# Kernel tuning notes

Measured on AMD Instinct MI355X. Metric: run time of the kernel, lower is better.

## Reference

```python
import jax, jax.numpy as jnp
import numpy as np

N4, N3, N2, N1, K = 32768, 65536, 131072, 262144, 16
G = 512


def _w(key, fan_in, fan_out):
    return jax.random.normal(key, (fan_in, fan_out), dtype=jnp.float32) / np.sqrt(fan_in)


def setup_inputs() -> dict:
    key = jax.random.key(0)
    ks = jax.random.split(key, 24)

    def edges(k, n_coarse, n_fine):
        # each fine (output) point gathers from K random coarse (input) points
        src = jax.random.randint(k, (n_fine * K,), 0, n_coarse, dtype=jnp.int32)
        dst = jnp.repeat(jnp.arange(n_fine, dtype=jnp.int32), K)
        return src, dst

    src3, dst3 = edges(ks[0], N4, N3)
    src2, dst2 = edges(ks[1], N3, N2)
    src1, dst1 = edges(ks[2], N2, N1)

    def gidx(k, n):
        return jnp.sort(jax.random.randint(k, (n,), 0, G, dtype=jnp.int32))

    inp = {
        'z_mask': jax.random.normal(ks[3], (N4, 64), dtype=jnp.float32),
        'pos4': jax.random.normal(ks[4], (N4, 3), dtype=jnp.float32),
        'pos3': jax.random.normal(ks[5], (N3, 3), dtype=jnp.float32),
        'pos2': jax.random.normal(ks[6], (N2, 3), dtype=jnp.float32),
        'pos1': jax.random.normal(ks[7], (N1, 3), dtype=jnp.float32),
        'g4': gidx(ks[8], N4), 'g3': gidx(ks[9], N3),
        'g2': gidx(ks[10], N2), 'g1': gidx(ks[11], N1),
        # PointConv MLP params: Linear(c_in+3 -> c_mid), CELU, Linear(c_mid -> c_out), max-aggregate
        'w1a': _w(ks[12], 64 + 3, 64), 'b1a': jnp.zeros((64,), jnp.float32),
        'w1b': _w(ks[13], 64, 32), 'b1b': jnp.zeros((32,), jnp.float32),
        'w2a': _w(ks[14], 32 + 3, 16), 'b2a': jnp.zeros((16,), jnp.float32),
        'w2b': _w(ks[15], 16, 16), 'b2b': jnp.zeros((16,), jnp.float32),
        'w3a': _w(ks[16], 16 + 3, 8), 'b3a': jnp.zeros((8,), jnp.float32),
        'w3b': _w(ks[17], 8, 8), 'b3b': jnp.zeros((8,), jnp.float32),
        'wlin': _w(ks[18], 8, 1), 'blin': jnp.zeros((1,), jnp.float32),
        'src3': src3, 'dst3': dst3,
        'src2': src2, 'dst2': dst2,
        'src1': src1, 'dst1': dst1,
    }
    return inp


def point_conv(x_in, pos_in, pos_out, src, dst, w_a, b_a, w_b, b_b, n_out):
    # gather: per-edge neighbor features + relative positions
    rel = pos_in[src] - pos_out[dst]                      # [E, 3]
    feat = jnp.concatenate([x_in[src], rel], axis=-1)     # [E, c_in+3]
    h = jax.nn.celu(feat @ w_a + b_a)                     # [E, c_mid]
    m = h @ w_b + b_b                                     # [E, c_out]
    # scatter: max-aggregate edge messages onto output points
    return jax.ops.segment_max(m, dst, num_segments=n_out)


def reference(z_mask, pos4, pos3, pos2, pos1, g4, g3, g2, g1,
              w1a, b1a, w1b, b1b, w2a, b2a, w2b, b2b, w3a, b3a, w3b, b3b,
              wlin, blin, src3, dst3, src2, dst2, src1, dst1):
    out = jax.nn.celu(point_conv(z_mask, pos4, pos3, src3, dst3, w1a, b1a, w1b, b1b, N3))
    out = jax.nn.celu(point_conv(out, pos3, pos2, src2, dst2, w2a, b2a, w2b, b2b, N2))
    out = jax.nn.celu(point_conv(out, pos2, pos1, src1, dst1, w3a, b3a, w3b, b3b, N1))
    logits = out @ wlin + blin                            # [N1, 1]
    return jax.nn.log_sigmoid(logits)
```

## Files before the change

kernel.cpp:

```cpp
#include <hip/hip_runtime.h>
#include <hip/hip_fp16.h>
#include <math.h>

#define N4C 32768
#define N3C 65536
#define N2C 131072
#define N1C 262144

typedef _Float16 f16x8 __attribute__((ext_vector_type(8)));
typedef float f32x4 __attribute__((ext_vector_type(4)));
typedef float f32x16 __attribute__((ext_vector_type(16)));

__device__ __forceinline__ f32x4 mfma16(f16x8 a, f16x8 b, f32x4 c) {
  return __builtin_amdgcn_mfma_f32_16x16x32_f16(a, b, c, 0, 0, 0);
}
__device__ __forceinline__ f32x16 mfma32(f16x8 a, f16x8 b, f32x16 c) {
  return __builtin_amdgcn_mfma_f32_32x32x16_f16(a, b, c, 0, 0, 0);
}

__device__ __forceinline__ float celuf(float x) {
  return fmaxf(x, 0.f) + (__expf(fminf(x, 0.f)) - 1.f);
}

__device__ __forceinline__ float logsigf(float x) {
  float e = __expf(-fabsf(x));
  return fminf(x, 0.f) - __logf(1.f + e);
}

__device__ __forceinline__ float max3f(float a, float b, float c) {
  return fmaxf(fmaxf(a, b), c);
}

__device__ __forceinline__ _Float16 exp2_16(_Float16 x) {
  __half h; __builtin_memcpy(&h, &x, 2);
  h = hexp2(h);
  _Float16 r; __builtin_memcpy(&r, &h, 2);
  return r;
}

__device__ __forceinline__ f16x8 celu8p1(f16x8 x) {
  f16x8 z = {};
  f16x8 mx = __builtin_elementwise_max(x, z);
  f16x8 mn = __builtin_elementwise_min(x, z) * (_Float16)1.44269504f;
#pragma unroll
  for (int i = 0; i < 8; ++i) mn[i] = exp2_16(mn[i]);
  return mx + mn;
}

__global__ __launch_bounds__(256) void y4_kernel(
    const float* __restrict__ z, const float* __restrict__ pos4,
    const float* __restrict__ pos3, const float* __restrict__ w1a,
    const float* __restrict__ b1a, _Float16* __restrict__ y4,
    _Float16* __restrict__ vt3) {
  if (blockIdx.x >= 512) {
    const int idx = (blockIdx.x - 512) * 256 + threadIdx.x;
    const int p = idx >> 3, seg = (idx & 7) * 8;
    const float q0 = pos3[p * 3 + 0];
    const float q1 = pos3[p * 3 + 1];
    const float q2 = pos3[p * 3 + 2];
    f16x8 v;
#pragma unroll
    for (int j = 0; j < 8; ++j) {
      const int k = seg + j;
      v[j] = (_Float16)(w1a[64 * 64 + k] * q0 + w1a[65 * 64 + k] * q1 +
                        w1a[66 * 64 + k] * q2);
    }
    *(f16x8*)(vt3 + (size_t)p * 64 + seg) = v;
    return;
  }
  const int lane = threadIdx.x & 63, wid = threadIdx.x >> 6;
  const int col = lane & 15, quad = lane >> 4;
  const int base = (blockIdx.x * 4 + wid) * 16;

  f16x8 Ba[2][4];
#pragma unroll
  for (int c = 0; c < 2; ++c)
#pragma unroll
    for (int t = 0; t < 4; ++t)
#pragma unroll
      for (int j = 0; j < 8; ++j)
        Ba[c][t][j] = (_Float16)w1a[(c * 32 + quad * 8 + j) * 64 + t * 16 + col];

  float wr[3][4];
#pragma unroll
  for (int c = 0; c < 3; ++c)
#pragma unroll
    for (int t = 0; t < 4; ++t)
      wr[c][t] = w1a[(64 + c) * 64 + t * 16 + col];

  float px[4], py[4], pz[4];
#pragma unroll
  for (int r = 0; r < 4; ++r) {
    const int row = base + quad * 4 + r;
    px[r] = pos4[row * 3 + 0];
    py[r] = pos4[row * 3 + 1];
    pz[r] = pos4[row * 3 + 2];
  }

  const float* zr = z + (size_t)(base + col) * 64;
  f16x8 A0, A1;
  {
    float4 f0 = *(const float4*)(zr + quad * 8);
    float4 f1 = *(const float4*)(zr + quad * 8 + 4);
    float4 f2 = *(const float4*)(zr + 32 + quad * 8);
    float4 f3 = *(const float4*)(zr + 32 + quad * 8 + 4);
    A0[0] = (_Float16)f0.x; A0[1] = (_Float16)f0.y; A0[2] = (_Float16)f0.z; A0[3] = (_Float16)f0.w;
    A0[4] = (_Float16)f1.x; A0[5] = (_Float16)f1.y; A0[6] = (_Float16)f1.z; A0[7] = (_Float16)f1.w;
    A1[0] = (_Float16)f2.x; A1[1] = (_Float16)f2.y; A1[2] = (_Float16)f2.z; A1[3] = (_Float16)f2.w;
    A1[4] = (_Float16)f3.x; A1[5] = (_Float16)f3.y; A1[6] = (_Float16)f3.z; A1[7] = (_Float16)f3.w;
  }
#pragma unroll
  for (int t = 0; t < 4; ++t) {
    f32x4 acc = {0.f, 0.f, 0.f, 0.f};
    acc = mfma16(A0, Ba[0][t], acc);
    acc = mfma16(A1, Ba[1][t], acc);
    const float bt = b1a[t * 16 + col];
#pragma unroll
    for (int r = 0; r < 4; ++r) {
      const float posterm =
          px[r] * wr[0][t] + py[r] * wr[1][t] + pz[r] * wr[2][t];
      y4[(size_t)(base + quad * 4 + r) * 64 + t * 16 + col] =
          (_Float16)(acc[r] + bt + posterm);
    }
  }
}

__global__ __launch_bounds__(256) void y3_kernel(
    const _Float16* __restrict__ x3f, const float* __restrict__ pos3,
    const float* __restrict__ pos2, const float* __restrict__ w2a,
    const float* __restrict__ b2a, _Float16* __restrict__ y3,
    _Float16* __restrict__ vt2) {
  if (blockIdx.x >= 1024) {
    const int idx = (blockIdx.x - 1024) * 256 + threadIdx.x;
    const int p = idx >> 1, seg = (idx & 1) * 8;
    const float q0 = pos2[p * 3 + 0];
    const float q1 = pos2[p * 3 + 1];
    const float q2 = pos2[p * 3 + 2];
    f16x8 v;
#pragma unroll
    for (int j = 0; j < 8; ++j) {
      const int k = seg + j;
      v[j] = (_Float16)(w2a[32 * 16 + k] * q0 + w2a[33 * 16 + k] * q1 +
                        w2a[34 * 16 + k] * q2);
    }
    *(f16x8*)(vt2 + (size_t)p * 16 + seg) = v;
    return;
  }
  const int lane = threadIdx.x & 63, wid = threadIdx.x >> 6;
  const int col = lane & 15, quad = lane >> 4;
  const int base = (blockIdx.x * 4 + wid) * 16;

  f16x8 B;
#pragma unroll
  for (int j = 0; j < 8; ++j) B[j] = (_Float16)w2a[(quad * 8 + j) * 16 + col];

  float wr[3];
#pragma unroll
  for (int c = 0; c < 3; ++c) wr[c] = w2a[(32 + c) * 16 + col];

  float px[4], py[4], pz[4];
#pragma unroll
  for (int r = 0; r < 4; ++r) {
    const int row = base + quad * 4 + r;
    px[r] = pos3[row * 3 + 0];
    py[r] = pos3[row * 3 + 1];
    pz[r] = pos3[row * 3 + 2];
  }

  f16x8 A = *(const f16x8*)(x3f + (size_t)(base + col) * 32 + quad * 8);
  f32x4 d = {0.f, 0.f, 0.f, 0.f};
  d = mfma16(A, B, d);
  const float bt = b2a[col];
#pragma unroll
  for (int r = 0; r < 4; ++r) {
    const float posterm = px[r] * wr[0] + py[r] * wr[1] + pz[r] * wr[2];
    y3[(size_t)(base + quad * 4 + r) * 16 + col] =
        (_Float16)(d[r] + bt + posterm);
  }
}

__global__ __launch_bounds__(256) void y2_kernel(
    const _Float16* __restrict__ x2f, const float* __restrict__ pos2,
    const float* __restrict__ pos1, const float* __restrict__ w3a,
    const float* __restrict__ b3a, _Float16* __restrict__ y2,
    _Float16* __restrict__ vt1) {
  if (blockIdx.x >= 2048) {
    const int p = (blockIdx.x - 2048) * 256 + threadIdx.x;
    const float q0 = pos1[p * 3 + 0];
    const float q1 = pos1[p * 3 + 1];
    const float q2 = pos1[p * 3 + 2];
    f16x8 v;
#pragma unroll
    for (int k = 0; k < 8; ++k)
      v[k] = (_Float16)(w3a[16 * 8 + k] * q0 + w3a[17 * 8 + k] * q1 +
                        w3a[18 * 8 + k] * q2);
    *(f16x8*)(vt1 + (size_t)p * 8) = v;
    return;
  }
  const int lane = threadIdx.x & 63, wid = threadIdx.x >> 6;
  const int col = lane & 15, quad = lane >> 4;
  const int base = (blockIdx.x * 4 + wid) * 16;

  f16x8 B;
#pragma unroll
  for (int j = 0; j < 8; ++j) {
    int k = quad * 8 + j;
    B[j] = (k < 16 && col < 8) ? (_Float16)w3a[k * 8 + col] : (_Float16)0.f;
  }
  f16x8 A = *(const f16x8*)(x2f + (size_t)(base + col) * 16 + (quad & 1) * 8);
  f32x4 d = {0.f, 0.f, 0.f, 0.f};
  d = mfma16(A, B, d);
  if (col < 8) {
    float wr[3];
#pragma unroll
    for (int c = 0; c < 3; ++c) wr[c] = w3a[(16 + c) * 8 + col];
    const float bt = b3a[col];
#pragma unroll
    for (int r = 0; r < 4; ++r) {
      const int row = base + quad * 4 + r;
      const float posterm = pos2[row * 3 + 0] * wr[0] +
                            pos2[row * 3 + 1] * wr[1] +
                            pos2[row * 3 + 2] * wr[2];
      y2[(size_t)row * 8 + col] = (_Float16)(d[r] + bt + posterm);
    }
  }
}

__global__ __launch_bounds__(256) void l3_kernel(
    const _Float16* __restrict__ y4, const _Float16* __restrict__ vt3,
    const int* __restrict__ src3, const float* __restrict__ w1b,
    const float* __restrict__ b1b, _Float16* __restrict__ x3f) {
  const int lane = threadIdx.x & 63, wid = threadIdx.x >> 6;
  const int n = lane & 31;
  const int kh = lane >> 5;

  f16x8 Bb[4];
#pragma unroll
  for (int ks = 0; ks < 4; ++ks)
#pragma unroll
    for (int j = 0; j < 8; ++j)
      Bb[ks][j] = (_Float16)w1b[(ks * 16 + kh * 8 + j) * 32 + n];

  float s = 0.f;
#pragma unroll 4
  for (int k = 0; k < 32; ++k) s += w1b[(kh * 32 + k) * 32 + n];
  s += __shfl_xor(s, 32, 64);
  const float biasB = b1b[n] - s;

  const int gwave = blockIdx.x * 4 + wid;
  const int nw = gridDim.x << 2;

#pragma unroll 1
  for (int pb = gwave * 2; pb < N3C; pb += nw * 2) {
    const int s1 = src3[pb * 16 + n];
    const int p = pb + (n >> 4);
    const _Float16* yrow = y4 + (size_t)s1 * 64 + kh * 8;
    const _Float16* vrow = vt3 + (size_t)p * 64 + kh * 8;

    f16x8 A[4];
#pragma unroll
    for (int ks = 0; ks < 4; ++ks)
      A[ks] = *(const f16x8*)(yrow + ks * 16) - *(const f16x8*)(vrow + ks * 16);
#pragma unroll
    for (int ks = 0; ks < 4; ++ks) A[ks] = celu8p1(A[ks]);

    f32x16 acc = {};
#pragma unroll
    for (int ks = 0; ks < 4; ++ks) acc = mfma32(A[ks], Bb[ks], acc);

    float mA = fmaxf(max3f(max3f(acc[0], acc[1], acc[2]),
                           max3f(acc[3], acc[4], acc[5]), acc[6]), acc[7]);
    float mB = fmaxf(max3f(max3f(acc[8], acc[9], acc[10]),
                           max3f(acc[11], acc[12], acc[13]), acc[14]), acc[15]);
    mA = fmaxf(mA, __shfl_xor(mA, 32, 64));
    mB = fmaxf(mB, __shfl_xor(mB, 32, 64));

    const float mv = kh ? mB : mA;
    x3f[(size_t)(pb + kh) * 32 + n] = (_Float16)celuf(mv + biasB);
  }
}

__device__ __forceinline__ void l2_compute(
    int pr, f16x8 A_in, f16x8 vt, f16x8 Bb, float biasB, int kh, int n,
    _Float16* __restrict__ x2f) {
  f16x8 A = celu8p1(A_in - vt);
  f32x16 acc = {};
  acc = mfma32(A, Bb, acc);

  float mA = fmaxf(max3f(max3f(acc[0], acc[1], acc[2]),
                         max3f(acc[3], acc[4], acc[5]), acc[6]), acc[7]);
  float mB = fmaxf(max3f(max3f(acc[8], acc[9], acc[10]),
                         max3f(acc[11], acc[12], acc[13]), acc[14]), acc[15]);
  mA = fmaxf(mA, __shfl_xor(mA, 32, 64));
  mB = fmaxf(mB, __shfl_xor(mB, 32, 64));

  if (n < 16) {
    const float m = kh ? mB : mA;
    x2f[(size_t)(2 * pr + kh) * 16 + n] = (_Float16)celuf(m + biasB);
  }
}

__global__ __launch_bounds__(256) void l2_kernel(
    const _Float16* __restrict__ y3, const _Float16* __restrict__ vt2,
    const int* __restrict__ src2, const float* __restrict__ w2b,
    const float* __restrict__ b2b, _Float16* __restrict__ x2f) {
  const int lane = threadIdx.x & 63, wid = threadIdx.x >> 6;
  const int n = lane & 31;
  const int e = lane & 15;
  const int h = (lane >> 4) & 1;
  const int kh = lane >> 5;

  f16x8 Bb;
#pragma unroll
  for (int j = 0; j < 8; ++j)
    Bb[j] = (n < 16) ? (_Float16)w2b[(kh * 8 + j) * 16 + n] : (_Float16)0.f;
  float ws = 0.f;
#pragma unroll
  for (int k = 0; k < 16; ++k) ws += w2b[k * 16 + (n & 15)];
  const float biasB = b2b[n & 15] - ws;

  const int gwave = blockIdx.x * 4 + wid;
  const int nw = gridDim.x << 2;

#pragma unroll 1
  for (int pr = gwave; pr < N2C / 2; pr += 2 * nw) {
    const int pr2 = pr + nw;
    const int pa = 2 * pr + h, pb = 2 * pr2 + h;
    const int sa = src2[pa * 16 + e];
    const int sb = src2[pb * 16 + e];

    f16x8 Aa = *(const f16x8*)(y3 + (size_t)sa * 16 + kh * 8);
    f16x8 Ab = *(const f16x8*)(y3 + (size_t)sb * 16 + kh * 8);
    f16x8 va = *(const f16x8*)(vt2 + (size_t)pa * 16 + kh * 8);
    f16x8 vb = *(const f16x8*)(vt2 + (size_t)pb * 16 + kh * 8);

    l2_compute(pr,  Aa, va, Bb, biasB, kh, n, x2f);
    l2_compute(pr2, Ab, vb, Bb, biasB, kh, n, x2f);
  }
}

__device__ __forceinline__ void l1_compute(
    int pb, f16x8 A_in, f16x8 vt, f16x8 Bb, float biasB, float wl, float bl,
    int lane, float* __restrict__ out) {
  f16x8 A = celu8p1(A_in - vt);
  f32x16 acc = {};
  acc = mfma32(A, Bb, acc);

  float mA = fmaxf(max3f(max3f(acc[0], acc[1], acc[2]),
                         max3f(acc[3], acc[4], acc[5]), acc[6]), acc[7]);
  float mB = fmaxf(max3f(max3f(acc[8], acc[9], acc[10]),
                         max3f(acc[11], acc[12], acc[13]), acc[14]), acc[15]);
  mA = fmaxf(mA, __shfl_xor(mA, 32, 64));
  mB = fmaxf(mB, __shfl_xor(mB, 32, 64));

  float tA = celuf(mA + biasB) * wl;
  float tB = celuf(mB + biasB) * wl;
  tA += __shfl_xor(tA, 1, 64);
  tA += __shfl_xor(tA, 2, 64);
  tA += __shfl_xor(tA, 4, 64);
  tB += __shfl_xor(tB, 1, 64);
  tB += __shfl_xor(tB, 2, 64);
  tB += __shfl_xor(tB, 4, 64);
  if (lane == 0) {
    float2 o; o.x = logsigf(tA + bl); o.y = logsigf(tB + bl);
    *(float2*)(out + pb) = o;
  } else if (lane == 8) {
    float2 o; o.x = logsigf(tA + bl); o.y = logsigf(tB + bl);
    *(float2*)(out + pb + 2) = o;
  }
}

__global__ __launch_bounds__(256) void l1_kernel(
    const _Float16* __restrict__ y2, const _Float16* __restrict__ vt1,
    const int* __restrict__ src1, const float* __restrict__ w3b,
    const float* __restrict__ b3b, const float* __restrict__ wlin,
    const float* __restrict__ blin, float* __restrict__ out) {
  const int lane = threadIdx.x & 63, wid = threadIdx.x >> 6;
  const int m = lane & 31;
  const int e = lane & 15;
  const int h = (lane >> 4) & 1;
  const int kh = lane >> 5;
  const int g = 2 * kh + h;

  f16x8 Bb;
  const int n = m;
#pragma unroll
  for (int j = 0; j < 8; ++j)
    Bb[j] = (n < 16 && (n >> 3) == kh) ? (_Float16)w3b[j * 8 + (n & 7)]
                                       : (_Float16)0.f;
  float ws = 0.f;
#pragma unroll
  for (int j = 0; j < 8; ++j) ws += w3b[j * 8 + (n & 7)];
  const float biasB = (n < 16) ? b3b[n & 7] - ws : 0.f;
  const float wl = (n < 16) ? wlin[n & 7] : 0.f;
  const float bl = blin[0];

  const int gwave = blockIdx.x * 4 + wid;
  const int nw = gridDim.x << 2;

#pragma unroll 1
  for (int q = gwave; q < N1C / 4; q += 2 * nw) {
    const int q2 = q + nw;
    const int pba = q * 4, pbb = q2 * 4;
    const int pa = pba + g, pb = pbb + g;
    const int sa = src1[pa * 16 + e];
    const int sb = src1[pb * 16 + e];

    f16x8 Aa = *(const f16x8*)(y2 + (size_t)sa * 8);
    f16x8 Ab = *(const f16x8*)(y2 + (size_t)sb * 8);
    f16x8 va = *(const f16x8*)(vt1 + (size_t)pa * 8);
    f16x8 vb = *(const f16x8*)(vt1 + (size_t)pb * 8);

    l1_compute(pba, Aa, va, Bb, biasB, wl, bl, lane, out);
    l1_compute(pbb, Ab, vb, Bb, biasB, wl, bl, lane, out);
  }
}

extern "C" void kernel_launch(void* const* d_in, const int* in_sizes, int n_in,
                              void* d_out, int out_size, void* d_ws, size_t ws_size,
                              hipStream_t stream) {
  const float* z_mask = (const float*)d_in[0];
  const float* pos4 = (const float*)d_in[1];
  const float* pos3 = (const float*)d_in[2];
  const float* pos2 = (const float*)d_in[3];
  const float* pos1 = (const float*)d_in[4];
  const float* w1a = (const float*)d_in[9];
  const float* b1a = (const float*)d_in[10];
  const float* w1b = (const float*)d_in[11];
  const float* b1b = (const float*)d_in[12];
  const float* w2a = (const float*)d_in[13];
  const float* b2a = (const float*)d_in[14];
  const float* w2b = (const float*)d_in[15];
  const float* b2b = (const float*)d_in[16];
  const float* w3a = (const float*)d_in[17];
  const float* b3a = (const float*)d_in[18];
  const float* w3b = (const float*)d_in[19];
  const float* b3b = (const float*)d_in[20];
  const float* wlin = (const float*)d_in[21];
  const float* blin = (const float*)d_in[22];
  const int* src3 = (const int*)d_in[23];
  const int* src2 = (const int*)d_in[25];
  const int* src1 = (const int*)d_in[27];

  char* w = (char*)d_ws;
  _Float16* y4  = (_Float16*)(w);
  _Float16* vt3 = (_Float16*)(w + (4u << 20));
  _Float16* x3f = (_Float16*)(w + (12u << 20));
  _Float16* y3  = (_Float16*)(w);
  _Float16* vt2 = (_Float16*)(w + (4u << 20));
  _Float16* x2f = (_Float16*)(w + (8u << 20));
  _Float16* y2  = (_Float16*)(w + (2u << 20));
  _Float16* vt1 = (_Float16*)(w + (12u << 20));
  float* out = (float*)d_out;

  y4_kernel<<<2560, 256, 0, stream>>>(z_mask, pos4, pos3, w1a, b1a, y4, vt3);
  l3_kernel<<<2048, 256, 0, stream>>>(y4, vt3, src3, w1b, b1b, x3f);
  y3_kernel<<<2048, 256, 0, stream>>>(x3f, pos3, pos2, w2a, b2a, y3, vt2);
  l2_kernel<<<2048, 256, 0, stream>>>(y3, vt2, src2, w2b, b2b, x2f);
  y2_kernel<<<3072, 256, 0, stream>>>(x2f, pos2, pos1, w3a, b3a, y2, vt1);
  l1_kernel<<<2048, 256, 0, stream>>>(y2, vt1, src1, w3b, b3b,
                                      wlin, blin, out);
}
```

Measured before the change: 235.0 us.

## Fuse next-layer first linear into aggregation kernels and hoist all vt precomputes

The separate y3 and y2 projection kernels are removed. Their first-layer linear is computed inside l3 and l2 by accumulating each wave's aggregated outputs into an MFMA through lane shuffles, and y3/y2 are written directly. The vt2/vt1 position precomputes move into the first kernel's grid, which cuts the launch count from six to four and removes the round trip through the intermediate x3f/x2f buffers. In exchange, the l3/l2 loops now assume a fixed iteration count tied to the grid size, and extra shuffles and MFMAs are added per iteration.

```diff
diff --git a/kernel.cpp b/kernel.cpp
--- a/kernel.cpp
+++ b/kernel.cpp
@@ -8,6 +8,7 @@
 #define N1C 262144
 
 typedef _Float16 f16x8 __attribute__((ext_vector_type(8)));
+typedef _Float16 f16x4 __attribute__((ext_vector_type(4)));
 typedef float f32x4 __attribute__((ext_vector_type(4)));
 typedef float f32x16 __attribute__((ext_vector_type(16)));
 
@@ -49,11 +50,44 @@
 
 __global__ __launch_bounds__(256) void y4_kernel(
     const float* __restrict__ z, const float* __restrict__ pos4,
-    const float* __restrict__ pos3, const float* __restrict__ w1a,
+    const float* __restrict__ pos3, const float* __restrict__ pos2,
+    const float* __restrict__ pos1, const float* __restrict__ w1a,
+    const float* __restrict__ w2a, const float* __restrict__ w3a,
     const float* __restrict__ b1a, _Float16* __restrict__ y4,
-    _Float16* __restrict__ vt3) {
-  if (blockIdx.x >= 512) {
-    const int idx = (blockIdx.x - 512) * 256 + threadIdx.x;
+    _Float16* __restrict__ vt3, _Float16* __restrict__ vt2,
+    _Float16* __restrict__ vt1) {
+  const int bx = blockIdx.x;
+  if (bx >= 3584) {
+    const int p = (bx - 3584) * 256 + threadIdx.x;
+    const float q0 = pos1[p * 3 + 0];
+    const float q1 = pos1[p * 3 + 1];
+    const float q2 = pos1[p * 3 + 2];
+    f16x8 v;
+#pragma unroll
+    for (int k = 0; k < 8; ++k)
+      v[k] = (_Float16)(w3a[16 * 8 + k] * q0 + w3a[17 * 8 + k] * q1 +
+                        w3a[18 * 8 + k] * q2);
+    *(f16x8*)(vt1 + (size_t)p * 8) = v;
+    return;
+  }
+  if (bx >= 2560) {
+    const int idx = (bx - 2560) * 256 + threadIdx.x;
+    const int p = idx >> 1, seg = (idx & 1) * 8;
+    const float q0 = pos2[p * 3 + 0];
+    const float q1 = pos2[p * 3 + 1];
+    const float q2 = pos2[p * 3 + 2];
+    f16x8 v;
+#pragma unroll
+    for (int j = 0; j < 8; ++j) {
+      const int k = seg + j;
+      v[j] = (_Float16)(w2a[32 * 16 + k] * q0 + w2a[33 * 16 + k] * q1 +
+                        w2a[34 * 16 + k] * q2);
+    }
+    *(f16x8*)(vt2 + (size_t)p * 16 + seg) = v;
+    return;
+  }
+  if (bx >= 512) {
+    const int idx = (bx - 512) * 256 + threadIdx.x;
     const int p = idx >> 3, seg = (idx & 7) * 8;
     const float q0 = pos3[p * 3 + 0];
     const float q1 = pos3[p * 3 + 1];
@@ -70,7 +104,7 @@
   }
   const int lane = threadIdx.x & 63, wid = threadIdx.x >> 6;
   const int col = lane & 15, quad = lane >> 4;
-  const int base = (blockIdx.x * 4 + wid) * 16;
+  const int base = (bx * 4 + wid) * 16;
 
   f16x8 Ba[2][4];
 #pragma unroll
@@ -125,114 +159,40 @@
   }
 }
 
-__global__ __launch_bounds__(256) void y3_kernel(
-    const _Float16* __restrict__ x3f, const float* __restrict__ pos3,
-    const float* __restrict__ pos2, const float* __restrict__ w2a,
-    const float* __restrict__ b2a, _Float16* __restrict__ y3,
-    _Float16* __restrict__ vt2) {
-  if (blockIdx.x >= 1024) {
-    const int idx = (blockIdx.x - 1024) * 256 + threadIdx.x;
-    const int p = idx >> 1, seg = (idx & 1) * 8;
-    const float q0 = pos2[p * 3 + 0];
-    const float q1 = pos2[p * 3 + 1];
-    const float q2 = pos2[p * 3 + 2];
-    f16x8 v;
-#pragma unroll
-    for (int j = 0; j < 8; ++j) {
-      const int k = seg + j;
-      v[j] = (_Float16)(w2a[32 * 16 + k] * q0 + w2a[33 * 16 + k] * q1 +
-                        w2a[34 * 16 + k] * q2);
-    }
-    *(f16x8*)(vt2 + (size_t)p * 16 + seg) = v;
-    return;
-  }
-  const int lane = threadIdx.x & 63, wid = threadIdx.x >> 6;
-  const int col = lane & 15, quad = lane >> 4;
-  const int base = (blockIdx.x * 4 + wid) * 16;
-
-  f16x8 B;
-#pragma unroll
-  for (int j = 0; j < 8; ++j) B[j] = (_Float16)w2a[(quad * 8 + j) * 16 + col];
-
-  float wr[3];
-#pragma unroll
-  for (int c = 0; c < 3; ++c) wr[c] = w2a[(32 + c) * 16 + col];
-
-  float px[4], py[4], pz[4];
-#pragma unroll
-  for (int r = 0; r < 4; ++r) {
-    const int row = base + quad * 4 + r;
-    px[r] = pos3[row * 3 + 0];
-    py[r] = pos3[row * 3 + 1];
-    pz[r] = pos3[row * 3 + 2];
-  }
-
-  f16x8 A = *(const f16x8*)(x3f + (size_t)(base + col) * 32 + quad * 8);
-  f32x4 d = {0.f, 0.f, 0.f, 0.f};
-  d = mfma16(A, B, d);
-  const float bt = b2a[col];
-#pragma unroll
-  for (int r = 0; r < 4; ++r) {
-    const float posterm = px[r] * wr[0] + py[r] * wr[1] + pz[r] * wr[2];
-    y3[(size_t)(base + quad * 4 + r) * 16 + col] =
-        (_Float16)(d[r] + bt + posterm);
-  }
-}
-
-__global__ __launch_bounds__(256) void y2_kernel(
-    const _Float16* __restrict__ x2f, const float* __restrict__ pos2,
-    const float* __restrict__ pos1, const float* __restrict__ w3a,
-    const float* __restrict__ b3a, _Float16* __restrict__ y2,
-    _Float16* __restrict__ vt1) {
-  if (blockIdx.x >= 2048) {
-    const int p = (blockIdx.x - 2048) * 256 + threadIdx.x;
-    const float q0 = pos1[p * 3 + 0];
-    const float q1 = pos1[p * 3 + 1];
-    const float q2 = pos1[p * 3 + 2];
-    f16x8 v;
-#pragma unroll
-    for (int k = 0; k < 8; ++k)
-      v[k] = (_Float16)(w3a[16 * 8 + k] * q0 + w3a[17 * 8 + k] * q1 +
-                        w3a[18 * 8 + k] * q2);
-    *(f16x8*)(vt1 + (size_t)p * 8) = v;
-    return;
-  }
-  const int lane = threadIdx.x & 63, wid = threadIdx.x >> 6;
-  const int col = lane & 15, quad = lane >> 4;
-  const int base = (blockIdx.x * 4 + wid) * 16;
-
-  f16x8 B;
+__device__ __forceinline__ void accum_y3(f32x4& acc3, f16x8 Af, float x,
+                                         int colr, int quad, int i) {
+  f16x8 Bf;
 #pragma unroll
   for (int j = 0; j < 8; ++j) {
-    int k = quad * 8 + j;
-    B[j] = (k < 16 && col < 8) ? (_Float16)w3a[k * 8 + col] : (_Float16)0.f;
-  }
-  f16x8 A = *(const f16x8*)(x2f + (size_t)(base + col) * 16 + (quad & 1) * 8);
-  f32x4 d = {0.f, 0.f, 0.f, 0.f};
-  d = mfma16(A, B, d);
-  if (col < 8) {
-    float wr[3];
-#pragma unroll
-    for (int c = 0; c < 3; ++c) wr[c] = w3a[(16 + c) * 8 + col];
-    const float bt = b3a[col];
-#pragma unroll
-    for (int r = 0; r < 4; ++r) {
-      const int row = base + quad * 4 + r;
-      const float posterm = pos2[row * 3 + 0] * wr[0] +
-                            pos2[row * 3 + 1] * wr[1] +
-                            pos2[row * 3 + 2] * wr[2];
-      y2[(size_t)row * 8 + col] = (_Float16)(d[r] + bt + posterm);
-    }
-  }
+    const int sl = ((colr & 1) << 5) + quad * 8 + j;
+    const float v = __shfl(x, sl, 64);
+    Bf[j] = ((colr >> 1) == i) ? (_Float16)v : (_Float16)0.f;
+  }
+  acc3 = mfma16(Af, Bf, acc3);
+}
+
+__device__ __forceinline__ void accum_y2(f32x4& acc2, f16x8 Af, float x,
+                                         int colr, int quad, int t) {
+  f16x8 Bf;
+#pragma unroll
+  for (int j = 0; j < 8; ++j) {
+    const int sl = ((colr & 1) << 5) + quad * 8 + j;
+    const float v = __shfl(x, sl, 64);
+    Bf[j] = (quad < 2 && (colr >> 1) == t) ? (_Float16)v : (_Float16)0.f;
+  }
+  acc2 = mfma16(Af, Bf, acc2);
 }
 
 __global__ __launch_bounds__(256) void l3_kernel(
     const _Float16* __restrict__ y4, const _Float16* __restrict__ vt3,
     const int* __restrict__ src3, const float* __restrict__ w1b,
-    const float* __restrict__ b1b, _Float16* __restrict__ x3f) {
+    const float* __restrict__ b1b, const float* __restrict__ pos3,
+    const float* __restrict__ w2a, const float* __restrict__ b2a,
+    _Float16* __restrict__ y3) {
   const int lane = threadIdx.x & 63, wid = threadIdx.x >> 6;
   const int n = lane & 31;
   const int kh = lane >> 5;
+  const int colr = lane & 15, quad = lane >> 4;
 
   f16x8 Bb[4];
 #pragma unroll
@@ -247,11 +207,18 @@
   s += __shfl_xor(s, 32, 64);
   const float biasB = b1b[n] - s;
 
+  f16x8 Af;
+#pragma unroll
+  for (int j = 0; j < 8; ++j)
+    Af[j] = (_Float16)w2a[(quad * 8 + j) * 16 + colr];
+  f32x4 acc3 = {0.f, 0.f, 0.f, 0.f};
+
   const int gwave = blockIdx.x * 4 + wid;
   const int nw = gridDim.x << 2;
 
 #pragma unroll 1
-  for (int pb = gwave * 2; pb < N3C; pb += nw * 2) {
+  for (int i = 0; i < 4; ++i) {
+    const int pb = 2 * gwave + 2 * nw * i;
     const int s1 = src3[pb * 16 + n];
     const int p = pb + (n >> 4);
     const _Float16* yrow = y4 + (size_t)s1 * 64 + kh * 8;
@@ -275,40 +242,39 @@
     mA = fmaxf(mA, __shfl_xor(mA, 32, 64));
     mB = fmaxf(mB, __shfl_xor(mB, 32, 64));
 
-    const float mv = kh ? mB : mA;
-    x3f[(size_t)(pb + kh) * 32 + n] = (_Float16)celuf(mv + biasB);
-  }
-}
-
-__device__ __forceinline__ void l2_compute(
-    int pr, f16x8 A_in, f16x8 vt, f16x8 Bb, float biasB, int kh, int n,
-    _Float16* __restrict__ x2f) {
-  f16x8 A = celu8p1(A_in - vt);
-  f32x16 acc = {};
-  acc = mfma32(A, Bb, acc);
-
-  float mA = fmaxf(max3f(max3f(acc[0], acc[1], acc[2]),
-                         max3f(acc[3], acc[4], acc[5]), acc[6]), acc[7]);
-  float mB = fmaxf(max3f(max3f(acc[8], acc[9], acc[10]),
-                         max3f(acc[11], acc[12], acc[13]), acc[14]), acc[15]);
-  mA = fmaxf(mA, __shfl_xor(mA, 32, 64));
-  mB = fmaxf(mB, __shfl_xor(mB, 32, 64));
-
-  if (n < 16) {
-    const float m = kh ? mB : mA;
-    x2f[(size_t)(2 * pr + kh) * 16 + n] = (_Float16)celuf(m + biasB);
+    const float x = (float)(_Float16)celuf((kh ? mB : mA) + biasB);
+    accum_y3(acc3, Af, x, colr, quad, i);
+  }
+
+  if (colr < 8) {
+    const int p = 2 * gwave + 2 * nw * (colr >> 1) + (colr & 1);
+    const float q0 = pos3[p * 3 + 0];
+    const float q1 = pos3[p * 3 + 1];
+    const float q2 = pos3[p * 3 + 2];
+    f16x4 o;
+#pragma unroll
+    for (int r = 0; r < 4; ++r) {
+      const int c = quad * 4 + r;
+      const float pt = q0 * w2a[32 * 16 + c] + q1 * w2a[33 * 16 + c] +
+                       q2 * w2a[34 * 16 + c];
+      o[r] = (_Float16)(acc3[r] + b2a[c] + pt);
+    }
+    *(f16x4*)(y3 + (size_t)p * 16 + quad * 4) = o;
   }
 }
 
 __global__ __launch_bounds__(256) void l2_kernel(
     const _Float16* __restrict__ y3, const _Float16* __restrict__ vt2,
     const int* __restrict__ src2, const float* __restrict__ w2b,
-    const float* __restrict__ b2b, _Float16* __restrict__ x2f) {
+    const float* __restrict__ b2b, const float* __restrict__ pos2,
+    const float* __restrict__ w3a, const float* __restrict__ b3a,
+    _Float16* __restrict__ y2) {
   const int lane = threadIdx.x & 63, wid = threadIdx.x >> 6;
   const int n = lane & 31;
   const int e = lane & 15;
   const int h = (lane >> 4) & 1;
   const int kh = lane >> 5;
+  const int colr = lane & 15, quad = lane >> 4;
 
   f16x8 Bb;
 #pragma unroll
@@ -319,11 +285,20 @@
   for (int k = 0; k < 16; ++k) ws += w2b[k * 16 + (n & 15)];
   const float biasB = b2b[n & 15] - ws;
 
+  f16x8 Af = {};
+#pragma unroll
+  for (int j = 0; j < 8; ++j) {
+    const int k = quad * 8 + j;
+    Af[j] = (k < 16 && colr < 8) ? (_Float16)w3a[k * 8 + colr] : (_Float16)0.f;
+  }
+  f32x4 acc2 = {0.f, 0.f, 0.f, 0.f};
+
   const int gwave = blockIdx.x * 4 + wid;
   const int nw = gridDim.x << 2;
 
 #pragma unroll 1
-  for (int pr = gwave; pr < N2C / 2; pr += 2 * nw) {
+  for (int i = 0; i < 4; ++i) {
+    const int pr = gwave + 2 * nw * i;
     const int pr2 = pr + nw;
     const int pa = 2 * pr + h, pb = 2 * pr2 + h;
     const int sa = src2[pa * 16 + e];
@@ -334,8 +309,42 @@
     f16x8 va = *(const f16x8*)(vt2 + (size_t)pa * 16 + kh * 8);
     f16x8 vb = *(const f16x8*)(vt2 + (size_t)pb * 16 + kh * 8);
 
-    l2_compute(pr,  Aa, va, Bb, biasB, kh, n, x2f);
-    l2_compute(pr2, Ab, vb, Bb, biasB, kh, n, x2f);
+#pragma unroll
+    for (int sub = 0; sub < 2; ++sub) {
+      const f16x8 A = celu8p1((sub ? Ab : Aa) - (sub ? vb : va));
+      f32x16 acc = {};
+      acc = mfma32(A, Bb, acc);
+
+      float mA = fmaxf(max3f(max3f(acc[0], acc[1], acc[2]),
+                             max3f(acc[3], acc[4], acc[5]), acc[6]), acc[7]);
+      float mB = fmaxf(max3f(max3f(acc[8], acc[9], acc[10]),
+                             max3f(acc[11], acc[12], acc[13]), acc[14]),
+                       acc[15]);
+      mA = fmaxf(mA, __shfl_xor(mA, 32, 64));
+      mB = fmaxf(mB, __shfl_xor(mB, 32, 64));
+
+      const float x = (float)(_Float16)celuf((kh ? mB : mA) + biasB);
+      accum_y2(acc2, Af, x, colr, quad, 2 * i + sub);
+    }
+  }
+
+  if (quad < 2) {
+    const int t = colr >> 1, kh2 = colr & 1;
+    const int it = t >> 1, sub = t & 1;
+    const int pr = gwave + 2 * nw * it + nw * sub;
+    const int p = 2 * pr + kh2;
+    const float q0 = pos2[p * 3 + 0];
+    const float q1 = pos2[p * 3 + 1];
+    const float q2 = pos2[p * 3 + 2];
+    f16x4 o;
+#pragma unroll
+    for (int r = 0; r < 4; ++r) {
+      const int c = quad * 4 + r;
+      const float pt = q0 * w3a[16 * 8 + c] + q1 * w3a[17 * 8 + c] +
+                       q2 * w3a[18 * 8 + c];
+      o[r] = (_Float16)(acc2[r] + b3a[c] + pt);
+    }
+    *(f16x4*)(y2 + (size_t)p * 8 + quad * 4) = o;
   }
 }
 
@@ -377,10 +386,8 @@
     const float* __restrict__ blin, float* __restrict__ out) {
   const int lane = threadIdx.x & 63, wid = threadIdx.x >> 6;
   const int m = lane & 31;
-  const int e = lane & 15;
-  const int h = (lane >> 4) & 1;
   const int kh = lane >> 5;
-  const int g = 2 * kh + h;
+  const int g = 2 * kh + ((lane >> 4) & 1);
 
   f16x8 Bb;
   const int n = m;
@@ -403,8 +410,8 @@
     const int q2 = q + nw;
     const int pba = q * 4, pbb = q2 * 4;
     const int pa = pba + g, pb = pbb + g;
-    const int sa = src1[pa * 16 + e];
-    const int sb = src1[pb * 16 + e];
+    const int sa = src1[q * 64 + lane];
+    const int sb = src1[q2 * 64 + lane];
 
     f16x8 Aa = *(const f16x8*)(y2 + (size_t)sa * 8);
     f16x8 Ab = *(const f16x8*)(y2 + (size_t)sb * 8);
@@ -445,19 +452,18 @@
   char* w = (char*)d_ws;
   _Float16* y4  = (_Float16*)(w);
   _Float16* vt3 = (_Float16*)(w + (4u << 20));
-  _Float16* x3f = (_Float16*)(w + (12u << 20));
-  _Float16* y3  = (_Float16*)(w);
-  _Float16* vt2 = (_Float16*)(w + (4u << 20));
-  _Float16* x2f = (_Float16*)(w + (8u << 20));
-  _Float16* y2  = (_Float16*)(w + (2u << 20));
-  _Float16* vt1 = (_Float16*)(w + (12u << 20));
+  _Float16* y3  = (_Float16*)(w + (12u << 20));
+  _Float16* y2  = (_Float16*)(w + (14u << 20));
+  _Float16* vt2 = (_Float16*)(w + (16u << 20));
+  _Float16* vt1 = (_Float16*)(w + (20u << 20));
   float* out = (float*)d_out;
 
-  y4_kernel<<<2560, 256, 0, stream>>>(z_mask, pos4, pos3, w1a, b1a, y4, vt3);
-  l3_kernel<<<2048, 256, 0, stream>>>(y4, vt3, src3, w1b, b1b, x3f);
-  y3_kernel<<<2048, 256, 0, stream>>>(x3f, pos3, pos2, w2a, b2a, y3, vt2);
-  l2_kernel<<<2048, 256, 0, stream>>>(y3, vt2, src2, w2b, b2b, x2f);
-  y2_kernel<<<3072, 256, 0, stream>>>(x2f, pos2, pos1, w3a, b3a, y2, vt1);
+  y4_kernel<<<4608, 256, 0, stream>>>(z_mask, pos4, pos3, pos2, pos1, w1a,
+                                      w2a, w3a, b1a, y4, vt3, vt2, vt1);
+  l3_kernel<<<2048, 256, 0, stream>>>(y4, vt3, src3, w1b, b1b, pos3, w2a,
+                                      b2a, y3);
+  l2_kernel<<<2048, 256, 0, stream>>>(y3, vt2, src2, w2b, b2b, pos2, w3a,
+                                      b3a, y2);
   l1_kernel<<<2048, 256, 0, stream>>>(y2, vt1, src1, w3b, b3b,
                                       wlin, blin, out);
 }
```

After: 234.2 us. About the same (-0.3%).
